# Kernel tuning notes

Measured on AMD Instinct MI355X. Metric: run time of the kernel, lower is better.

## Reference

```python
import jax, jax.numpy as jnp
import numpy as np
import math

GROUPS = 32
EPS = 1e-5

def group_norm(x, w, b):
    B, C, H, W = x.shape
    xg = x.reshape(B, GROUPS, C // GROUPS, H, W)
    mu = xg.mean(axis=(2, 3, 4), keepdims=True)
    var = xg.var(axis=(2, 3, 4), keepdims=True)
    xn = ((xg - mu) * jax.lax.rsqrt(var + EPS)).reshape(B, C, H, W)
    return xn * w[None, :, None, None] + b[None, :, None, None]

def conv1x1(x, w, b):
    # x: [B,Cin,H,W], w: [Cout,Cin], b: [Cout]
    return jnp.einsum('bchw,oc->bohw', x, w) + b[None, :, None, None]

def setup_inputs() -> dict:
    key = jax.random.key(0)
    ks = jax.random.split(key, 8)
    B, C, E, H, W = 8, 256, 512, 64, 64
    x = jax.random.normal(ks[0], (B, C, H, W), dtype=jnp.float32)
    condA = jax.random.normal(ks[1], (B, E, H, W), dtype=jnp.float32)
    gn_x_w = jnp.ones((C,), jnp.float32)
    gn_x_b = jnp.zeros((C,), jnp.float32)
    gn_c_w = jnp.ones((E,), jnp.float32)
    gn_c_b = jnp.zeros((E,), jnp.float32)
    q_w = jax.random.normal(ks[2], (C, C), jnp.float32) * 0.02
    q_b = jnp.zeros((C,), jnp.float32)
    k_w = jax.random.normal(ks[3], (C, E), jnp.float32) * 0.02
    k_b = jnp.zeros((C,), jnp.float32)
    v_w = jax.random.normal(ks[4], (C, E), jnp.float32) * 0.02
    v_b = jnp.zeros((C,), jnp.float32)
    return {"x": x, "condA": condA, "gn_x_w": gn_x_w, "gn_x_b": gn_x_b,
            "gn_c_w": gn_c_w, "gn_c_b": gn_c_b, "q_w": q_w, "q_b": q_b,
            "k_w": k_w, "k_b": k_b, "v_w": v_w, "v_b": v_b}

def reference(x, condA, gn_x_w, gn_x_b, gn_c_w, gn_c_b, q_w, q_b, k_w, k_b, v_w, v_b):
    B, C, H, W = x.shape
    scale = math.sqrt(C)
    h = group_norm(x, gn_x_w, gn_x_b)
    h1 = group_norm(condA, gn_c_w, gn_c_b)
    q = conv1x1(h, q_w, q_b)      # [B,C,H,W]
    k = conv1x1(h1, k_w, k_b)     # [B,C,Hc,Wc]
    v = conv1x1(h1, v_w, v_b)     # [B,C,Hc,Wc]
    qf = q.transpose(0, 2, 3, 1).reshape(B, H * W, C)        # [B,N,C]
    kf = k.reshape(B, C, -1)                                  # [B,C,M]
    vf = v.transpose(0, 2, 3, 1).reshape(B, -1, C)            # [B,M,C]
    attn = jax.nn.softmax(jnp.einsum('bnc,bcm->bnm', qf, kf) / scale, axis=-1)
    out = jnp.einsum('bnm,bmc->bnc', attn, vf)                # [B,N,C]
    return out.reshape(B, H, W, C).transpose(0, 3, 1, 2)
```

## Files before the change

kernel.cpp:

```cpp
#include <hip/hip_runtime.h>


typedef _Float16 half8 __attribute__((ext_vector_type(8)));
typedef _Float16 half4v __attribute__((ext_vector_type(4)));
typedef float f32x4 __attribute__((ext_vector_type(4)));
typedef float f32x16 __attribute__((ext_vector_type(16)));

#define MFMA16(a, b, c) __builtin_amdgcn_mfma_f32_16x16x32_f16((a), (b), (c), 0, 0, 0)
#define MFMA32(a, b, c) __builtin_amdgcn_mfma_f32_32x32x16_f16((a), (b), (c), 0, 0, 0)

__global__ __launch_bounds__(256) void statswconv_kernel(
    const float* __restrict__ x, const float* __restrict__ condA,
    float* __restrict__ sx, float* __restrict__ sc,
    const float* __restrict__ wq, const float* __restrict__ wk,
    const float* __restrict__ wv, _Float16* __restrict__ wqt,
    _Float16* __restrict__ wkt, _Float16* __restrict__ wvt) {
  int bid = blockIdx.x;
  int t = threadIdx.x;
  if (bid >= 512) {
    int i = (bid - 512) * 256 + t;
    const float* src;
    _Float16* dst;
    int cin, ksbits, gi;
    if (i < 8192) { src = wq; dst = wqt; cin = 256; ksbits = 3; gi = i; }
    else if (i < 24576) { src = wk; dst = wkt; cin = 512; ksbits = 4; gi = i - 8192; }
    else { src = wv; dst = wvt; cin = 512; ksbits = 4; gi = i - 24576; }
    int tile = gi >> 6, g = gi & 63;
    int otile = tile >> ksbits, ks = tile & ((1 << ksbits) - 1);
    int o = otile * 16 + (g & 15), k = ks * 32 + (g >> 4) * 8;
    const float* s = src + (size_t)o * cin + k;
    half8 hv;
#pragma unroll
    for (int j = 0; j < 8; j++) hv[j] = (_Float16)s[j];
    *(half8*)(dst + (size_t)gi * 8) = hv;
    return;
  }
  const float4* src;
  int nf4;
  float* dst;
  float inv_n;
  if (bid < 256) {
    src = (const float4*)(x + (size_t)bid * 32768);
    nf4 = 8192;
    dst = sx + bid * 2;
    inv_n = 1.0f / 32768.0f;
  } else {
    int j = bid - 256;
    src = (const float4*)(condA + (size_t)j * 65536);
    nf4 = 16384;
    dst = sc + j * 2;
    inv_n = 1.0f / 65536.0f;
  }
  float s = 0.f, s2 = 0.f;
  for (int i = t; i < nf4; i += 256) {
    float4 v = src[i];
    s += v.x + v.y + v.z + v.w;
    s2 += v.x * v.x + v.y * v.y + v.z * v.z + v.w * v.w;
  }
#pragma unroll
  for (int m = 1; m <= 32; m <<= 1) {
    s += __shfl_xor(s, m, 64);
    s2 += __shfl_xor(s2, m, 64);
  }
  __shared__ float red[8];
  int w = t >> 6;
  if ((t & 63) == 0) { red[w * 2] = s; red[w * 2 + 1] = s2; }
  __syncthreads();
  if (t == 0) {
    float S = red[0] + red[2] + red[4] + red[6];
    float S2 = red[1] + red[3] + red[5] + red[7];
    float mu = S * inv_n;
    float var = S2 * inv_n - mu * mu;
    dst[0] = mu;
    dst[1] = rsqrtf(var + 1e-5f);
  }
}

__global__ __launch_bounds__(256) void ntrans_kernel(
    const float* __restrict__ x, const float* __restrict__ condA,
    const float* __restrict__ statsx, const float* __restrict__ statsc,
    const float* __restrict__ gxw, const float* __restrict__ gxb,
    const float* __restrict__ gcw, const float* __restrict__ gcb,
    _Float16* __restrict__ hxTt, _Float16* __restrict__ h1Tt) {
  int bid = blockIdx.x;
  const float *src, *stats, *gw, *gb;
  _Float16* dst;
  int CH, gsh, bid2;
  if (bid < 2048) {
    src = x; stats = statsx; gw = gxw; gb = gxb; dst = hxTt;
    CH = 256; gsh = 3; bid2 = bid;
  } else {
    src = condA; stats = statsc; gw = gcw; gb = gcb; dst = h1Tt;
    CH = 512; gsh = 4; bid2 = bid - 2048;
  }
  int b = bid2 & 7, nt = (bid2 >> 3) & 63, ctile = bid2 >> 9;
  int n0 = nt * 64, c0 = ctile * 64;
  int t = threadIdx.x;
  __shared__ float tile[64][65];

  int cl = t >> 2;
  int c = c0 + cl;
  const float* st = stats + ((size_t)b * 32 + (c >> gsh)) * 2;
  float mu = st[0], rs = st[1];
  float a = rs * gw[c];
  float bb = gb[c] - mu * a;
  const float* srow = src + ((size_t)(b * CH + c)) * 4096 + n0 + (t & 3) * 16;
#pragma unroll
  for (int i = 0; i < 4; i++) {
    float4 v = *(const float4*)(srow + 4 * i);
    int nn = (t & 3) * 16 + 4 * i;
    tile[cl][nn + 0] = v.x * a + bb;
    tile[cl][nn + 1] = v.y * a + bb;
    tile[cl][nn + 2] = v.z * a + bb;
    tile[cl][nn + 3] = v.w * a + bb;
  }
  __syncthreads();
  int nl = t >> 2;
  half8 ov[2];
#pragma unroll
  for (int u = 0; u < 2; u++)
#pragma unroll
    for (int i = 0; i < 8; i++) ov[u][i] = (_Float16)tile[(t & 3) * 16 + 8 * u + i][nl];
  int n = n0 + nl;
  size_t tb = ((size_t)b * 256 + (n >> 4)) * (CH >> 5);
  int ca = c0 + (t & 3) * 16;
#pragma unroll
  for (int u = 0; u < 2; u++) {
    int cc = ca + 8 * u;
    size_t addr = ((tb + (cc >> 5)) * 64 + (n & 15) + 16 * ((cc >> 3) & 3)) * 8;
    *(half8*)(dst + addr) = ov[u];
  }
}

__global__ __launch_bounds__(256, 2) void projQ_kernel(
    const _Float16* __restrict__ Ht, const _Float16* __restrict__ Wt,
    const float* __restrict__ bias, _Float16* __restrict__ Qt) {
  int bid = blockIdx.x;
  int b = bid & 7, nt = bid >> 3;
  int t = threadIdx.x, l = t & 63, w = t >> 6;
  int c15 = l & 15, q = l >> 4;

  __shared__ __align__(16) _Float16 hbuf[16384];
  half8* hb = (half8*)hbuf;
  {
    const half8* sg = (const half8*)Ht + (size_t)(b * 256 + nt * 4) * 512;
#pragma unroll
    for (int i = 0; i < 8; i++) hb[t + 256 * i] = sg[t + 256 * i];
  }
  __syncthreads();

  const half8* wt8 = (const half8*)Wt;
#pragma unroll
  for (int p = 0; p < 2; p++) {
    int oa = (p * 4 + w) * 2;
    f32x4 acc[2][4] = {};
#pragma unroll
    for (int ks = 0; ks < 8; ks++) {
      half8 af0 = wt8[((size_t)(oa + 0) * 8 + ks) * 64 + l];
      half8 af1 = wt8[((size_t)(oa + 1) * 8 + ks) * 64 + l];
#pragma unroll
      for (int nt2 = 0; nt2 < 4; nt2++) {
        half8 bf = hb[(nt2 * 8 + ks) * 64 + l];
        acc[0][nt2] = MFMA16(af0, bf, acc[0][nt2]);
        acc[1][nt2] = MFMA16(af1, bf, acc[1][nt2]);
      }
    }
#pragma unroll
    for (int j = 0; j < 2; j++) {
      int o4 = (oa + j) * 16 + 4 * q;
      f32x4 bv = *(const f32x4*)(bias + o4);
#pragma unroll
      for (int nt2 = 0; nt2 < 4; nt2++) {
        half4v hv;
#pragma unroll
        for (int r = 0; r < 4; r++) hv[r] = (_Float16)((acc[j][nt2][r] + bv[r]) * 0.0625f);
        size_t addr = ((((size_t)b * 128 + nt * 2 + (nt2 >> 1)) * 16 + (oa + j)) * 64 +
                       (nt2 & 1) * 16 + c15 + 32 * (q >> 1)) * 8 + (q & 1) * 4;
        *(half4v*)(Qt + addr) = hv;
      }
    }
  }
}

__global__ __launch_bounds__(256, 2) void projKV_kernel(
    const _Float16* __restrict__ Ht, const _Float16* __restrict__ Wk,
    const _Float16* __restrict__ Wv, const float* __restrict__ kb,
    const float* __restrict__ vb, _Float16* __restrict__ Kt,
    _Float16* __restrict__ Vt) {
  int bid = blockIdx.x;
  int b = bid & 7, mt = bid >> 3;
  int m0 = mt * 64;
  int t = threadIdx.x, l = t & 63, w = t >> 6;
  int c15 = l & 15, q = l >> 4;

  __shared__ __align__(16) _Float16 hbuf[32768];
  half8* hb = (half8*)hbuf;
  {
    const half8* sg = (const half8*)Ht + (size_t)(b * 256 + mt * 4) * 1024;
#pragma unroll
    for (int i = 0; i < 16; i++) hb[t + 256 * i] = sg[t + 256 * i];
  }
  __syncthreads();

  const half8* wk8 = (const half8*)Wk;
  const half8* wv8 = (const half8*)Wv;
#pragma unroll
  for (int p = 0; p < 2; p++) {
    int oa = (p * 4 + w) * 2;
    f32x4 acck[2][4] = {};
    f32x4 accv[4][2] = {};
#pragma unroll
    for (int ks = 0; ks < 16; ks++) {
      half8 kf0 = wk8[((size_t)(oa + 0) * 16 + ks) * 64 + l];
      half8 kf1 = wk8[((size_t)(oa + 1) * 16 + ks) * 64 + l];
      half8 vf0 = wv8[((size_t)(oa + 0) * 16 + ks) * 64 + l];
      half8 vf1 = wv8[((size_t)(oa + 1) * 16 + ks) * 64 + l];
#pragma unroll
      for (int nt2 = 0; nt2 < 4; nt2++) {
        half8 lf = hb[(nt2 * 16 + ks) * 64 + l];
        acck[0][nt2] = MFMA16(kf0, lf, acck[0][nt2]);
        acck[1][nt2] = MFMA16(kf1, lf, acck[1][nt2]);
        accv[nt2][0] = MFMA16(lf, vf0, accv[nt2][0]);
        accv[nt2][1] = MFMA16(lf, vf1, accv[nt2][1]);
      }
    }
#pragma unroll
    for (int j = 0; j < 2; j++) {
      int o4 = (oa + j) * 16 + 4 * q;
      f32x4 bv = *(const f32x4*)(kb + o4);
#pragma unroll
      for (int nt2 = 0; nt2 < 4; nt2++) {
        half4v hv;
#pragma unroll
        for (int r = 0; r < 4; r++) hv[r] = (_Float16)(acck[j][nt2][r] + bv[r]);
        size_t addr = ((((size_t)b * 128 + mt * 2 + (nt2 >> 1)) * 16 + (oa + j)) * 64 +
                       (nt2 & 1) * 16 + c15 + 32 * (q >> 1)) * 8 + (q & 1) * 4;
        *(half4v*)(Kt + addr) = hv;
      }
    }
#pragma unroll
    for (int nt2 = 0; nt2 < 4; nt2++) {
      int m = m0 + nt2 * 16 + 4 * q;
      size_t mbase = ((size_t)b * 256 + (m >> 4)) * 8;
#pragma unroll
      for (int j = 0; j < 2; j++) {
        int c = (oa + j) * 16 + c15;
        float bs = vb[c];
        half4v hv;
#pragma unroll
        for (int r = 0; r < 4; r++) hv[r] = (_Float16)(accv[nt2][j][r] + bs);
        size_t addr = ((mbase + (c >> 5)) * 64 + (c & 31) + ((q >> 1) << 5)) * 8 + (q & 1) * 4;
        *(half4v*)(Vt + addr) = hv;
      }
    }
  }
}

__global__ __launch_bounds__(256, 2) void attn_kernel(
    const _Float16* __restrict__ Qt, const _Float16* __restrict__ Kt,
    const _Float16* __restrict__ Vt, float* __restrict__ out) {
  int bid = blockIdx.x;
  int b = bid & 7, nt = bid >> 3;
  int n0 = nt * 64;
  int t = threadIdx.x, l = t & 63, w = t >> 6;
  int l31 = l & 31, h = l >> 5;
  int mh = w & 1, nh = w >> 1;

  __shared__ __align__(16) _Float16 kbuf[16384];
  __shared__ __align__(16) _Float16 pbuf[4096];
  __shared__ float lsw[2][64];
  half8* kb8 = (half8*)kbuf;

  half8 qf[16];
  {
    const half8* qt8 = (const half8*)Qt + ((size_t)(b * 128 + nt * 2 + nh) * 16) * 64 + l;
#pragma unroll
    for (int ks = 0; ks < 16; ks++) qf[ks] = qt8[ks * 64];
  }

  const half8* ktb = (const half8*)Kt + (size_t)b * 131072 + t;
  const half8* vt8 = (const half8*)Vt + (size_t)b * 256 * 8 * 64;
  int gb = (l31 ^ h) | (h << 5);

  f32x16 acc_o[4] = {};
  float l_part = 0.f;

  half8 kreg[8];
#pragma unroll
  for (int i = 0; i < 8; i++) kreg[i] = ktb[256 * i];
#pragma unroll
  for (int i = 0; i < 8; i++) kb8[t + 256 * i] = kreg[i];
  __syncthreads();

  for (int it = 0; it < 64; it++) {
    int itn = it < 63 ? it + 1 : 63;
#pragma unroll
    for (int i = 0; i < 8; i++) kreg[i] = ktb[itn * 2048 + 256 * i];
    half8 vf0[8];
#pragma unroll
    for (int u = 0; u < 2; u++)
#pragma unroll
      for (int ct = 0; ct < 4; ct++)
        vf0[u * 4 + ct] = vt8[((size_t)(it * 4 + u) * 8 + (mh * 4 + ct)) * 64 + l];

    f32x16 s = {};
#pragma unroll
    for (int ks = 0; ks < 16; ks++) {
      half8 kf = kb8[(mh * 16 + ks) * 64 + l];
      s = MFMA32(kf, qf[ks], s);
    }

    half4v pv[4];
#pragma unroll
    for (int k2 = 0; k2 < 4; k2++) {
#pragma unroll
      for (int r = 0; r < 4; r++) {
        float e = __expf(s[4 * k2 + r]);
        l_part += e;
        pv[k2][r] = (_Float16)e;
      }
    }
    __syncthreads();

#pragma unroll
    for (int k2 = 0; k2 < 4; k2++) {
      int hm = k2 & 1;
      int tau = nh * 4 + mh * 2 + (k2 >> 1);
      int g = (l31 ^ hm) | (hm << 5);
      *(half4v*)&pbuf[tau * 512 + g * 8 + 4 * h] = pv[k2];
    }
#pragma unroll
    for (int i = 0; i < 8; i++) kb8[t + 256 * i] = kreg[i];
    __syncthreads();

    half8 vf1[8];
#pragma unroll
    for (int u = 0; u < 2; u++)
#pragma unroll
      for (int ct = 0; ct < 4; ct++)
        vf1[u * 4 + ct] = vt8[((size_t)(it * 4 + 2 + u) * 8 + (mh * 4 + ct)) * 64 + l];
#pragma unroll
    for (int ks = 0; ks < 2; ks++) {
      half8 pf = *(const half8*)&pbuf[(nh * 4 + ks) * 512 + gb * 8];
#pragma unroll
      for (int ct = 0; ct < 4; ct++) acc_o[ct] = MFMA32(pf, vf0[ks * 4 + ct], acc_o[ct]);
    }
#pragma unroll
    for (int ks = 2; ks < 4; ks++) {
      half8 pf = *(const half8*)&pbuf[(nh * 4 + ks) * 512 + gb * 8];
#pragma unroll
      for (int ct = 0; ct < 4; ct++) acc_o[ct] = MFMA32(pf, vf1[(ks - 2) * 4 + ct], acc_o[ct]);
    }
  }

  {
    float v = l_part + __shfl_xor(l_part, 32, 64);
    if (l < 32) lsw[mh][nh * 32 + l] = v;
  }
  __syncthreads();
#pragma unroll
  for (int k2 = 0; k2 < 4; k2++) {
    int nb = nh * 32 + 4 * h + 8 * k2;
    f32x4 s0 = *(const f32x4*)&lsw[0][nb];
    f32x4 s1 = *(const f32x4*)&lsw[1][nb];
    f32x4 linv;
#pragma unroll
    for (int r = 0; r < 4; r++) linv[r] = 1.0f / (s0[r] + s1[r]);
#pragma unroll
    for (int ct = 0; ct < 4; ct++) {
      int c = mh * 128 + ct * 32 + l31;
      f32x4 o4;
#pragma unroll
      for (int r = 0; r < 4; r++) o4[r] = acc_o[ct][4 * k2 + r] * linv[r];
      *(f32x4*)(out + ((size_t)(b * 256 + c)) * 4096 + n0 + nb) = o4;
    }
  }
}

extern "C" void kernel_launch(void* const* d_in, const int* in_sizes, int n_in,
                              void* d_out, int out_size, void* d_ws,
                              size_t ws_size, hipStream_t stream) {
  const float* x = (const float*)d_in[0];
  const float* condA = (const float*)d_in[1];
  const float* gxw = (const float*)d_in[2];
  const float* gxb = (const float*)d_in[3];
  const float* gcw = (const float*)d_in[4];
  const float* gcb = (const float*)d_in[5];
  const float* qw = (const float*)d_in[6];
  const float* qb = (const float*)d_in[7];
  const float* kw = (const float*)d_in[8];
  const float* kb = (const float*)d_in[9];
  const float* vw = (const float*)d_in[10];
  const float* vb = (const float*)d_in[11];
  float* out = (float*)d_out;

  char* ws = (char*)d_ws;
  float* statsx = (float*)(ws);
  float* statsc = (float*)(ws + 2048);
  _Float16* wqt = (_Float16*)(ws + 4096);
  _Float16* wkt = (_Float16*)(ws + 135168);
  _Float16* wvt = (_Float16*)(ws + 397312);
  char* p = ws + 659456;
  _Float16* hxTt = (_Float16*)p; p += (size_t)8 * 4096 * 256 * 2;
  _Float16* h1Tt = (_Float16*)p; p += (size_t)8 * 4096 * 512 * 2;
  _Float16* Qt = (_Float16*)p;   p += (size_t)8 * 4096 * 256 * 2;
  _Float16* Kt = (_Float16*)p;   p += (size_t)8 * 4096 * 256 * 2;
  _Float16* Vt = (_Float16*)p;

  statswconv_kernel<<<672, 256, 0, stream>>>(x, condA, statsx, statsc,
                                             qw, kw, vw, wqt, wkt, wvt);
  ntrans_kernel<<<6144, 256, 0, stream>>>(x, condA, statsx, statsc,
                                          gxw, gxb, gcw, gcb, hxTt, h1Tt);
  projQ_kernel<<<512, 256, 0, stream>>>(hxTt, wqt, qb, Qt);
  projKV_kernel<<<512, 256, 0, stream>>>(h1Tt, wkt, wvt, kb, vb, Kt, Vt);
  attn_kernel<<<512, 256, 0, stream>>>(Qt, Kt, Vt, out);
}
```

Measured before the change: 393.6 us.

## Restructure attention with async LDS K double-buffering and register P shuffles; merge projections

The attention kernel now double-buffers K tiles in LDS using direct global-to-LDS loads, which removes the register staging and one barrier per iteration. It keeps P in registers through cross-lane shuffles instead of an LDS round trip. Each wave now accumulates all 256 output channels over half of the M range, and the two halves are summed in LDS at the end. The Q and KV projection kernels are merged into one launch to save launch overhead and let the two halves overlap. In exchange, the attention kernel uses more accumulator registers and more LDS, which may lower occupancy.

```diff
diff --git a/kernel.cpp b/kernel.cpp
--- a/kernel.cpp
+++ b/kernel.cpp
@@ -3,11 +3,20 @@
 
 typedef _Float16 half8 __attribute__((ext_vector_type(8)));
 typedef _Float16 half4v __attribute__((ext_vector_type(4)));
+typedef _Float16 half16 __attribute__((ext_vector_type(16)));
 typedef float f32x4 __attribute__((ext_vector_type(4)));
 typedef float f32x16 __attribute__((ext_vector_type(16)));
+typedef unsigned u32x8 __attribute__((ext_vector_type(8)));
+typedef unsigned u32x4 __attribute__((ext_vector_type(4)));
 
 #define MFMA16(a, b, c) __builtin_amdgcn_mfma_f32_16x16x32_f16((a), (b), (c), 0, 0, 0)
 #define MFMA32(a, b, c) __builtin_amdgcn_mfma_f32_32x32x16_f16((a), (b), (c), 0, 0, 0)
+
+__device__ __forceinline__ void gload_lds16(const void* g, void* l) {
+  __builtin_amdgcn_global_load_lds(
+      (const __attribute__((address_space(1))) unsigned int*)g,
+      (__attribute__((address_space(3))) unsigned int*)l, 16, 0, 0);
+}
 
 __global__ __launch_bounds__(256) void statswconv_kernel(
     const float* __restrict__ x, const float* __restrict__ condA,
@@ -132,76 +141,69 @@
   }
 }
 
-__global__ __launch_bounds__(256, 2) void projQ_kernel(
-    const _Float16* __restrict__ Ht, const _Float16* __restrict__ Wt,
-    const float* __restrict__ bias, _Float16* __restrict__ Qt) {
-  int bid = blockIdx.x;
-  int b = bid & 7, nt = bid >> 3;
+__global__ __launch_bounds__(256, 2) void projQKV_kernel(
+    const _Float16* __restrict__ HxT, const _Float16* __restrict__ H1T,
+    const _Float16* __restrict__ Wq, const _Float16* __restrict__ Wk,
+    const _Float16* __restrict__ Wv, const float* __restrict__ qb,
+    const float* __restrict__ kb, const float* __restrict__ vb,
+    _Float16* __restrict__ Qt, _Float16* __restrict__ Kt,
+    _Float16* __restrict__ Vt) {
+  __shared__ __align__(16) _Float16 hbuf[32768];
+  half8* hb = (half8*)hbuf;
   int t = threadIdx.x, l = t & 63, w = t >> 6;
   int c15 = l & 15, q = l >> 4;
 
-  __shared__ __align__(16) _Float16 hbuf[16384];
-  half8* hb = (half8*)hbuf;
-  {
-    const half8* sg = (const half8*)Ht + (size_t)(b * 256 + nt * 4) * 512;
-#pragma unroll
-    for (int i = 0; i < 8; i++) hb[t + 256 * i] = sg[t + 256 * i];
-  }
-  __syncthreads();
-
-  const half8* wt8 = (const half8*)Wt;
-#pragma unroll
-  for (int p = 0; p < 2; p++) {
-    int oa = (p * 4 + w) * 2;
-    f32x4 acc[2][4] = {};
-#pragma unroll
-    for (int ks = 0; ks < 8; ks++) {
-      half8 af0 = wt8[((size_t)(oa + 0) * 8 + ks) * 64 + l];
-      half8 af1 = wt8[((size_t)(oa + 1) * 8 + ks) * 64 + l];
-#pragma unroll
-      for (int nt2 = 0; nt2 < 4; nt2++) {
-        half8 bf = hb[(nt2 * 8 + ks) * 64 + l];
-        acc[0][nt2] = MFMA16(af0, bf, acc[0][nt2]);
-        acc[1][nt2] = MFMA16(af1, bf, acc[1][nt2]);
-      }
-    }
-#pragma unroll
-    for (int j = 0; j < 2; j++) {
-      int o4 = (oa + j) * 16 + 4 * q;
-      f32x4 bv = *(const f32x4*)(bias + o4);
-#pragma unroll
-      for (int nt2 = 0; nt2 < 4; nt2++) {
-        half4v hv;
-#pragma unroll
-        for (int r = 0; r < 4; r++) hv[r] = (_Float16)((acc[j][nt2][r] + bv[r]) * 0.0625f);
-        size_t addr = ((((size_t)b * 128 + nt * 2 + (nt2 >> 1)) * 16 + (oa + j)) * 64 +
-                       (nt2 & 1) * 16 + c15 + 32 * (q >> 1)) * 8 + (q & 1) * 4;
-        *(half4v*)(Qt + addr) = hv;
-      }
-    }
-  }
-}
-
-__global__ __launch_bounds__(256, 2) void projKV_kernel(
-    const _Float16* __restrict__ Ht, const _Float16* __restrict__ Wk,
-    const _Float16* __restrict__ Wv, const float* __restrict__ kb,
-    const float* __restrict__ vb, _Float16* __restrict__ Kt,
-    _Float16* __restrict__ Vt) {
-  int bid = blockIdx.x;
+  if (blockIdx.x < 512) {
+    int bid = blockIdx.x;
+    int b = bid & 7, nt = bid >> 3;
+    {
+      const half8* sg = (const half8*)HxT + (size_t)(b * 256 + nt * 4) * 512;
+#pragma unroll
+      for (int i = 0; i < 8; i++) hb[t + 256 * i] = sg[t + 256 * i];
+    }
+    __syncthreads();
+    const half8* wt8 = (const half8*)Wq;
+#pragma unroll
+    for (int p = 0; p < 2; p++) {
+      int oa = (p * 4 + w) * 2;
+      f32x4 acc[2][4] = {};
+#pragma unroll
+      for (int ks = 0; ks < 8; ks++) {
+        half8 af0 = wt8[((size_t)(oa + 0) * 8 + ks) * 64 + l];
+        half8 af1 = wt8[((size_t)(oa + 1) * 8 + ks) * 64 + l];
+#pragma unroll
+        for (int nt2 = 0; nt2 < 4; nt2++) {
+          half8 bf = hb[(nt2 * 8 + ks) * 64 + l];
+          acc[0][nt2] = MFMA16(af0, bf, acc[0][nt2]);
+          acc[1][nt2] = MFMA16(af1, bf, acc[1][nt2]);
+        }
+      }
+#pragma unroll
+      for (int j = 0; j < 2; j++) {
+        int o4 = (oa + j) * 16 + 4 * q;
+        f32x4 bv = *(const f32x4*)(qb + o4);
+#pragma unroll
+        for (int nt2 = 0; nt2 < 4; nt2++) {
+          half4v hv;
+#pragma unroll
+          for (int r = 0; r < 4; r++) hv[r] = (_Float16)((acc[j][nt2][r] + bv[r]) * 0.0625f);
+          size_t addr = ((((size_t)b * 128 + nt * 2 + (nt2 >> 1)) * 16 + (oa + j)) * 64 +
+                         (nt2 & 1) * 16 + c15 + 32 * (q >> 1)) * 8 + (q & 1) * 4;
+          *(half4v*)(Qt + addr) = hv;
+        }
+      }
+    }
+    return;
+  }
+  int bid = blockIdx.x - 512;
   int b = bid & 7, mt = bid >> 3;
   int m0 = mt * 64;
-  int t = threadIdx.x, l = t & 63, w = t >> 6;
-  int c15 = l & 15, q = l >> 4;
-
-  __shared__ __align__(16) _Float16 hbuf[32768];
-  half8* hb = (half8*)hbuf;
   {
-    const half8* sg = (const half8*)Ht + (size_t)(b * 256 + mt * 4) * 1024;
+    const half8* sg = (const half8*)H1T + (size_t)(b * 256 + mt * 4) * 1024;
 #pragma unroll
     for (int i = 0; i < 16; i++) hb[t + 256 * i] = sg[t + 256 * i];
   }
   __syncthreads();
-
   const half8* wk8 = (const half8*)Wk;
   const half8* wv8 = (const half8*)Wv;
 #pragma unroll
@@ -266,10 +268,8 @@
   int l31 = l & 31, h = l >> 5;
   int mh = w & 1, nh = w >> 1;
 
-  __shared__ __align__(16) _Float16 kbuf[16384];
-  __shared__ __align__(16) _Float16 pbuf[4096];
+  __shared__ __align__(16) _Float16 kbuf[2][16384];
   __shared__ float lsw[2][64];
-  half8* kb8 = (half8*)kbuf;
 
   half8 qf[16];
   {
@@ -278,101 +278,110 @@
     for (int ks = 0; ks < 16; ks++) qf[ks] = qt8[ks * 64];
   }
 
-  const half8* ktb = (const half8*)Kt + (size_t)b * 131072 + t;
-  const half8* vt8 = (const half8*)Vt + (size_t)b * 256 * 8 * 64;
-  int gb = (l31 ^ h) | (h << 5);
-
-  f32x16 acc_o[4] = {};
+  const half8* ktb = (const half8*)Kt + (size_t)b * 131072;
+  const half8* vt8 = (const half8*)Vt + (size_t)b * 131072;
+
+  f32x16 acc[8] = {};
   float l_part = 0.f;
 
-  half8 kreg[8];
-#pragma unroll
-  for (int i = 0; i < 8; i++) kreg[i] = ktb[256 * i];
-#pragma unroll
-  for (int i = 0; i < 8; i++) kb8[t + 256 * i] = kreg[i];
+  {
+    const half8* g = ktb + t;
+    _Float16* d = kbuf[0] + t * 8;
+#pragma unroll
+    for (int i = 0; i < 8; i++) gload_lds16(g + i * 256, d + i * 2048);
+  }
   __syncthreads();
 
   for (int it = 0; it < 64; it++) {
-    int itn = it < 63 ? it + 1 : 63;
-#pragma unroll
-    for (int i = 0; i < 8; i++) kreg[i] = ktb[itn * 2048 + 256 * i];
-    half8 vf0[8];
-#pragma unroll
-    for (int u = 0; u < 2; u++)
-#pragma unroll
-      for (int ct = 0; ct < 4; ct++)
-        vf0[u * 4 + ct] = vt8[((size_t)(it * 4 + u) * 8 + (mh * 4 + ct)) * 64 + l];
+    const half8* cur = (const half8*)kbuf[it & 1];
+    if (it < 63) {
+      const half8* g = ktb + (it + 1) * 2048 + t;
+      _Float16* d = kbuf[(it + 1) & 1] + t * 8;
+#pragma unroll
+      for (int i = 0; i < 8; i++) gload_lds16(g + i * 256, d + i * 2048);
+    }
+    half8 vf[8];
+#pragma unroll
+    for (int ct = 0; ct < 8; ct++)
+      vf[ct] = vt8[((size_t)(it * 4 + mh * 2) * 8 + ct) * 64 + l];
 
     f32x16 s = {};
 #pragma unroll
     for (int ks = 0; ks < 16; ks++) {
-      half8 kf = kb8[(mh * 16 + ks) * 64 + l];
+      half8 kf = cur[(mh * 16 + ks) * 64 + l];
       s = MFMA32(kf, qf[ks], s);
     }
 
-    half4v pv[4];
-#pragma unroll
-    for (int k2 = 0; k2 < 4; k2++) {
-#pragma unroll
-      for (int r = 0; r < 4; r++) {
-        float e = __expf(s[4 * k2 + r]);
-        l_part += e;
-        pv[k2][r] = (_Float16)e;
-      }
-    }
+    half16 ph;
+#pragma unroll
+    for (int r = 0; r < 16; r++) {
+      float e = __expf(s[r]);
+      l_part += e;
+      ph[r] = (_Float16)e;
+    }
+    u32x8 pu = __builtin_bit_cast(u32x8, ph);
+
+    half8 pf[2];
+#pragma unroll
+    for (int c2 = 0; c2 < 2; c2++) {
+      unsigned s0 = h ? pu[c2 * 4 + 0] : pu[c2 * 4 + 2];
+      unsigned s1 = h ? pu[c2 * 4 + 1] : pu[c2 * 4 + 3];
+      unsigned r0 = __shfl_xor(s0, 32, 64);
+      unsigned r1 = __shfl_xor(s1, 32, 64);
+      u32x4 fr;
+      fr[0] = h ? r0 : pu[c2 * 4 + 0];
+      fr[1] = h ? r1 : pu[c2 * 4 + 1];
+      fr[2] = h ? pu[c2 * 4 + 2] : r0;
+      fr[3] = h ? pu[c2 * 4 + 3] : r1;
+      pf[c2] = __builtin_bit_cast(half8, fr);
+    }
+
+#pragma unroll
+    for (int ct = 0; ct < 8; ct++) acc[ct] = MFMA32(pf[0], vf[ct], acc[ct]);
+#pragma unroll
+    for (int ct = 0; ct < 8; ct++)
+      vf[ct] = vt8[((size_t)(it * 4 + mh * 2 + 1) * 8 + ct) * 64 + l];
+#pragma unroll
+    for (int ct = 0; ct < 8; ct++) acc[ct] = MFMA32(pf[1], vf[ct], acc[ct]);
+
     __syncthreads();
-
-#pragma unroll
-    for (int k2 = 0; k2 < 4; k2++) {
-      int hm = k2 & 1;
-      int tau = nh * 4 + mh * 2 + (k2 >> 1);
-      int g = (l31 ^ hm) | (hm << 5);
-      *(half4v*)&pbuf[tau * 512 + g * 8 + 4 * h] = pv[k2];
-    }
-#pragma unroll
-    for (int i = 0; i < 8; i++) kb8[t + 256 * i] = kreg[i];
-    __syncthreads();
-
-    half8 vf1[8];
-#pragma unroll
-    for (int u = 0; u < 2; u++)
-#pragma unroll
-      for (int ct = 0; ct < 4; ct++)
-        vf1[u * 4 + ct] = vt8[((size_t)(it * 4 + 2 + u) * 8 + (mh * 4 + ct)) * 64 + l];
-#pragma unroll
-    for (int ks = 0; ks < 2; ks++) {
-      half8 pf = *(const half8*)&pbuf[(nh * 4 + ks) * 512 + gb * 8];
-#pragma unroll
-      for (int ct = 0; ct < 4; ct++) acc_o[ct] = MFMA32(pf, vf0[ks * 4 + ct], acc_o[ct]);
-    }
-#pragma unroll
-    for (int ks = 2; ks < 4; ks++) {
-      half8 pf = *(const half8*)&pbuf[(nh * 4 + ks) * 512 + gb * 8];
-#pragma unroll
-      for (int ct = 0; ct < 4; ct++) acc_o[ct] = MFMA32(pf, vf1[(ks - 2) * 4 + ct], acc_o[ct]);
-    }
   }
 
   {
     float v = l_part + __shfl_xor(l_part, 32, 64);
     if (l < 32) lsw[mh][nh * 32 + l] = v;
   }
+  float* red = (float*)kbuf;
+  if (mh == 1) {
+#pragma unroll
+    for (int ct = 0; ct < 8; ct++)
+#pragma unroll
+      for (int k2 = 0; k2 < 4; k2++) {
+        f32x4 v4;
+#pragma unroll
+        for (int r = 0; r < 4; r++) v4[r] = acc[ct][4 * k2 + r];
+        *(f32x4*)&red[nh * 8192 + ((ct * 4 + k2) * 64 + l) * 4] = v4;
+      }
+  }
   __syncthreads();
-#pragma unroll
-  for (int k2 = 0; k2 < 4; k2++) {
-    int nb = nh * 32 + 4 * h + 8 * k2;
-    f32x4 s0 = *(const f32x4*)&lsw[0][nb];
-    f32x4 s1 = *(const f32x4*)&lsw[1][nb];
-    f32x4 linv;
-#pragma unroll
-    for (int r = 0; r < 4; r++) linv[r] = 1.0f / (s0[r] + s1[r]);
-#pragma unroll
-    for (int ct = 0; ct < 4; ct++) {
-      int c = mh * 128 + ct * 32 + l31;
-      f32x4 o4;
-#pragma unroll
-      for (int r = 0; r < 4; r++) o4[r] = acc_o[ct][4 * k2 + r] * linv[r];
-      *(f32x4*)(out + ((size_t)(b * 256 + c)) * 4096 + n0 + nb) = o4;
+  if (mh == 0) {
+#pragma unroll
+    for (int k2 = 0; k2 < 4; k2++) {
+      int nb = nh * 32 + 4 * h + 8 * k2;
+      f32x4 s0 = *(const f32x4*)&lsw[0][nb];
+      f32x4 s1 = *(const f32x4*)&lsw[1][nb];
+      f32x4 linv;
+#pragma unroll
+      for (int r = 0; r < 4; r++) linv[r] = 1.0f / (s0[r] + s1[r]);
+#pragma unroll
+      for (int ct = 0; ct < 8; ct++) {
+        int c = ct * 32 + l31;
+        f32x4 ov = *(const f32x4*)&red[nh * 8192 + ((ct * 4 + k2) * 64 + l) * 4];
+        f32x4 o4;
+#pragma unroll
+        for (int r = 0; r < 4; r++) o4[r] = (acc[ct][4 * k2 + r] + ov[r]) * linv[r];
+        *(f32x4*)(out + ((size_t)(b * 256 + c)) * 4096 + n0 + nb) = o4;
+      }
     }
   }
 }
@@ -411,7 +420,7 @@
                                              qw, kw, vw, wqt, wkt, wvt);
   ntrans_kernel<<<6144, 256, 0, stream>>>(x, condA, statsx, statsc,
                                           gxw, gxb, gcw, gcb, hxTt, h1Tt);
-  projQ_kernel<<<512, 256, 0, stream>>>(hxTt, wqt, qb, Qt);
-  projKV_kernel<<<512, 256, 0, stream>>>(h1Tt, wkt, wvt, kb, vb, Kt, Vt);
+  projQKV_kernel<<<1024, 256, 0, stream>>>(hxTt, h1Tt, wqt, wkt, wvt,
+                                           qb, kb, vb, Qt, Kt, Vt);
   attn_kernel<<<512, 256, 0, stream>>>(Qt, Kt, Vt, out);
 }
```

Result: slower. 406.1 us (+3.2%).
